# Optimization experiments

Hardware: AMD Instinct MI355X
Metric: run time of the kernel (lower is better)

Reference implementation:

```python
import jax, jax.numpy as jnp
import numpy as np

RAD = 0.15          # sphere radius (init kwarg)
MIN_DIST = 2.0 * RAD  # two spheres collide when center distance < 2*rad


def setup_inputs() -> dict:
    key = jax.random.key(0)
    pos = jax.random.normal(key, (64, 1024, 3), dtype=jnp.float32)  # [T, N, 3]
    return {"pos": pos}


def reference(pos):
    """Sphere collision check equivalent to the sweep-and-prune CUDA kernel.

    The CUDA kernel sorts along one axis purely as an acceleration structure;
    the math it computes is: over all unordered robot pairs (i<j) at each
    timestep, a pair collides if ||p_i - p_j|| < 2*rad. Returns
      count: total number of colliding pairs (int)
      loss:  sum over colliding pairs of (2*rad - dist)^2 penetration penalty
    """
    T, N, _ = pos.shape
    diff = pos[:, :, None, :] - pos[:, None, :, :]          # [T, N, N, 3]
    dist2 = jnp.sum(diff * diff, axis=-1)                   # [T, N, N]
    iu = jnp.triu(jnp.ones((N, N), dtype=bool), k=1)        # i < j, exclude self
    colliding = iu[None, :, :] & (dist2 < MIN_DIST * MIN_DIST)
    # safe sqrt (diagonal / coincident points have dist2 == 0)
    safe_d2 = jnp.where(dist2 > 0.0, dist2, 1.0)
    dist = jnp.sqrt(safe_d2)
    pen = MIN_DIST - dist                                   # penetration depth
    loss = jnp.sum(jnp.where(colliding, pen * pen, 0.0))
    count = jnp.sum(colliding).astype(jnp.int32)
    return (count, loss)
```

## Files before the change

### kernel.cpp

```cpp
#include <hip/hip_runtime.h>
#include <math.h>

#define TN     64
#define NP     1024
#define RADIUS 0.15f
#define MIN_D  (2.0f * RADIUS)
#define R2     (MIN_D * MIN_D)

#define SPLIT  16
#define GI     16
#define NGRP   (NP / GI)
#define GPB    (NGRP / SPLIT)
#define BLOCK  256
#define NBLK   (TN * SPLIT)

__launch_bounds__(BLOCK, 4)
__global__ void collide_kernel(const float* __restrict__ pos,
                               float* __restrict__ partial) {
    __shared__ float sh[NP * 3];
    const int t     = blockIdx.x / SPLIT;
    const int split = blockIdx.x % SPLIT;
    const int tid   = threadIdx.x;

    const float4* p4  = (const float4*)(pos + (size_t)t * NP * 3);
    float4*       sh4 = (float4*)sh;
    #pragma unroll
    for (int i = 0; i < (NP * 3 / 4) / BLOCK; ++i)
        sh4[tid + i * BLOCK] = p4[tid + i * BLOCK];
    __syncthreads();

    unsigned int cnt = 0;
    float loss = 0.0f;

    #pragma unroll
    for (int m = 0; m < GPB; ++m) {
        const int g = (m & 1) ? (m * SPLIT + (SPLIT - 1 - split))
                              : (m * SPLIT + split);
        const int b = g * GI;

        float xi[GI], yi[GI], zi[GI];
        #pragma unroll
        for (int k = 0; k < GI; ++k) {
            xi[k] = sh[3 * (b + k) + 0];
            yi[k] = sh[3 * (b + k) + 1];
            zi[k] = sh[3 * (b + k) + 2];
        }
        #pragma unroll
        for (int k = 0; k < GI; ++k)
            asm volatile("" : "+v"(xi[k]), "+v"(yi[k]), "+v"(zi[k]));

        if (tid < GI - 1) {
            const int j = b + 1 + tid;
            const float xj = sh[3 * j], yj = sh[3 * j + 1], zj = sh[3 * j + 2];
            #pragma unroll
            for (int k = 0; k < GI; ++k) {
                if (k <= tid) {
                    const float dx = xi[k] - xj;
                    const float dy = yi[k] - yj;
                    const float dz = zi[k] - zj;
                    const float d2 = dx * dx + dy * dy + dz * dz;
                    if (d2 < R2) {
                        cnt++;
                        const float pen = MIN_D - __builtin_amdgcn_sqrtf(d2);
                        loss += pen * pen;
                    }
                }
            }
        }

        for (int j = b + GI + tid; j < NP; j += BLOCK) {
            const float xj = sh[3 * j], yj = sh[3 * j + 1], zj = sh[3 * j + 2];
            #pragma unroll
            for (int k = 0; k < GI; ++k) {
                const float dx = xi[k] - xj;
                const float dy = yi[k] - yj;
                const float dz = zi[k] - zj;
                const float d2 = dx * dx + dy * dy + dz * dz;
                const bool hit = d2 < R2;
                cnt += hit ? 1u : 0u;
                if (hit) {
                    const float pen = MIN_D - __builtin_amdgcn_sqrtf(d2);
                    loss += pen * pen;
                }
            }
        }
    }

    float fcnt = (float)cnt;
    #pragma unroll
    for (int off = 32; off > 0; off >>= 1) {
        fcnt += __shfl_down(fcnt, off);
        loss += __shfl_down(loss, off);
    }
    __shared__ float cs[BLOCK / 64], ls[BLOCK / 64];
    const int wave = tid >> 6;
    if ((tid & 63) == 0) { cs[wave] = fcnt; ls[wave] = loss; }
    __syncthreads();
    if (tid == 0) {
        float c = 0.0f, l = 0.0f;
        #pragma unroll
        for (int w = 0; w < BLOCK / 64; ++w) { c += cs[w]; l += ls[w]; }
        partial[2 * blockIdx.x + 0] = c;
        partial[2 * blockIdx.x + 1] = l;
    }
}

__global__ void finalize_kernel(const float* __restrict__ partial,
                                float* __restrict__ out) {
    const int tid = threadIdx.x;
    float c = 0.0f, l = 0.0f;
    #pragma unroll
    for (int i = 0; i < NBLK / BLOCK; ++i) {
        const float2 p = ((const float2*)partial)[tid + i * BLOCK];
        c += p.x;
        l += p.y;
    }
    #pragma unroll
    for (int off = 32; off > 0; off >>= 1) {
        c += __shfl_down(c, off);
        l += __shfl_down(l, off);
    }
    __shared__ float cs[BLOCK / 64], ls[BLOCK / 64];
    const int wave = tid >> 6;
    if ((tid & 63) == 0) { cs[wave] = c; ls[wave] = l; }
    __syncthreads();
    if (tid == 0) {
        float ct = 0.0f, lt = 0.0f;
        #pragma unroll
        for (int w = 0; w < BLOCK / 64; ++w) { ct += cs[w]; lt += ls[w]; }
        out[0] = ct;
        out[1] = lt;
    }
}

extern "C" void kernel_launch(void* const* d_in, const int* in_sizes, int n_in,
                              void* d_out, int out_size, void* d_ws, size_t ws_size,
                              hipStream_t stream) {
    const float* pos     = (const float*)d_in[0];
    float*       partial = (float*)d_ws;
    float*       out     = (float*)d_out;

    collide_kernel<<<NBLK, BLOCK, 0, stream>>>(pos, partial);
    finalize_kernel<<<1, BLOCK, 0, stream>>>(partial, out);
}
```

Before: 73.68 us.

## Bin-sort spheres along x and prune pair checks to neighboring bins

```diff
diff --git a/kernel.cpp b/kernel.cpp
--- a/kernel.cpp
+++ b/kernel.cpp
@@ -7,54 +7,102 @@
 #define MIN_D  (2.0f * RADIUS)
 #define R2     (MIN_D * MIN_D)
 
-#define SPLIT  16
+#define BLOCK  512
+#define WAVES  (BLOCK / 64)
+#define SPLIT  8
 #define GI     16
 #define NGRP   (NP / GI)
-#define GPB    (NGRP / SPLIT)
-#define BLOCK  256
 #define NBLK   (TN * SPLIT)
+#define PPT    (NP / BLOCK)
+
+#define NB     40
+#define XMIN   (-6.0f)
+#define INVW   3.3f
 
 __launch_bounds__(BLOCK, 4)
 __global__ void collide_kernel(const float* __restrict__ pos,
-                               float* __restrict__ partial) {
-    __shared__ float sh[NP * 3];
+                               double* __restrict__ partial) {
+    __shared__ float         shin[NP * 3];
+    __shared__ float         shs [NP * 3];
+    __shared__ unsigned int  hist[NB];
+    __shared__ unsigned int  S[NB + 1];
+    __shared__ unsigned char sbin[NP];
+
     const int t     = blockIdx.x / SPLIT;
     const int split = blockIdx.x % SPLIT;
     const int tid   = threadIdx.x;
+    const int lane  = tid & 63;
+    const int wave  = tid >> 6;
 
     const float4* p4  = (const float4*)(pos + (size_t)t * NP * 3);
-    float4*       sh4 = (float4*)sh;
-    #pragma unroll
-    for (int i = 0; i < (NP * 3 / 4) / BLOCK; ++i)
-        sh4[tid + i * BLOCK] = p4[tid + i * BLOCK];
+    float4*       sh4 = (float4*)shin;
+    for (int i = tid; i < NP * 3 / 4; i += BLOCK) sh4[i] = p4[i];
+    if (tid < NB) hist[tid] = 0u;
     __syncthreads();
 
-    unsigned int cnt = 0;
-    float loss = 0.0f;
+    int          bq[PPT];
+    unsigned int rq[PPT];
+    #pragma unroll
+    for (int q = 0; q < PPT; ++q) {
+        const int p = tid + q * BLOCK;
+        const float x = shin[3 * p];
+        int b = (int)((x - XMIN) * INVW);
+        b = b < 0 ? 0 : (b > NB - 1 ? NB - 1 : b);
+        bq[q] = b;
+        rq[q] = atomicAdd(&hist[b], 1u);
+    }
+    __syncthreads();
+
+    if (tid < 64) {
+        unsigned int c    = (tid < NB) ? hist[tid] : 0u;
+        unsigned int incl = c;
+        #pragma unroll
+        for (int d = 1; d < 64; d <<= 1) {
+            const unsigned int y = __shfl_up(incl, d, 64);
+            if (lane >= d) incl += y;
+        }
+        if (tid < NB) S[tid + 1] = incl;
+        if (tid == 0) S[0] = 0u;
+    }
+    __syncthreads();
 
     #pragma unroll
-    for (int m = 0; m < GPB; ++m) {
-        const int g = (m & 1) ? (m * SPLIT + (SPLIT - 1 - split))
-                              : (m * SPLIT + split);
+    for (int q = 0; q < PPT; ++q) {
+        const int p = tid + q * BLOCK;
+        const unsigned int dst = S[bq[q]] + rq[q];
+        shs[3 * dst + 0] = shin[3 * p + 0];
+        shs[3 * dst + 1] = shin[3 * p + 1];
+        shs[3 * dst + 2] = shin[3 * p + 2];
+        sbin[dst] = (unsigned char)bq[q];
+    }
+    __syncthreads();
+
+    unsigned int cnt  = 0;
+    double       loss = 0.0;
+    {
+        const int g = wave * SPLIT + split;
         const int b = g * GI;
 
         float xi[GI], yi[GI], zi[GI];
         #pragma unroll
         for (int k = 0; k < GI; ++k) {
-            xi[k] = sh[3 * (b + k) + 0];
-            yi[k] = sh[3 * (b + k) + 1];
-            zi[k] = sh[3 * (b + k) + 2];
+            xi[k] = shs[3 * (b + k) + 0];
+            yi[k] = shs[3 * (b + k) + 1];
+            zi[k] = shs[3 * (b + k) + 2];
         }
         #pragma unroll
         for (int k = 0; k < GI; ++k)
             asm volatile("" : "+v"(xi[k]), "+v"(yi[k]), "+v"(zi[k]));
 
-        if (tid < GI - 1) {
-            const int j = b + 1 + tid;
-            const float xj = sh[3 * j], yj = sh[3 * j + 1], zj = sh[3 * j + 2];
+        const int bb   = (int)sbin[b + GI - 1];
+        const int jend = (int)S[(bb + 2 <= NB) ? (bb + 2) : NB];
+
+        if (lane < GI - 1) {
+            const int j = b + 1 + lane;
+            const float xj = shs[3 * j], yj = shs[3 * j + 1], zj = shs[3 * j + 2];
             #pragma unroll
             for (int k = 0; k < GI; ++k) {
-                if (k <= tid) {
+                if (k <= lane) {
                     const float dx = xi[k] - xj;
                     const float dy = yi[k] - yj;
                     const float dz = zi[k] - zj;
@@ -62,14 +110,14 @@
                     if (d2 < R2) {
                         cnt++;
                         const float pen = MIN_D - __builtin_amdgcn_sqrtf(d2);
-                        loss += pen * pen;
+                        loss += (double)(pen * pen);
                     }
                 }
             }
         }
 
-        for (int j = b + GI + tid; j < NP; j += BLOCK) {
-            const float xj = sh[3 * j], yj = sh[3 * j + 1], zj = sh[3 * j + 2];
+        for (int j = b + GI + lane; j < jend; j += 64) {
+            const float xj = shs[3 * j], yj = shs[3 * j + 1], zj = shs[3 * j + 2];
             #pragma unroll
             for (int k = 0; k < GI; ++k) {
                 const float dx = xi[k] - xj;
@@ -80,7 +128,7 @@
                 cnt += hit ? 1u : 0u;
                 if (hit) {
                     const float pen = MIN_D - __builtin_amdgcn_sqrtf(d2);
-                    loss += pen * pen;
+                    loss += (double)(pen * pen);
                 }
             }
         }
@@ -92,26 +140,25 @@
         fcnt += __shfl_down(fcnt, off);
         loss += __shfl_down(loss, off);
     }
-    __shared__ float cs[BLOCK / 64], ls[BLOCK / 64];
-    const int wave = tid >> 6;
-    if ((tid & 63) == 0) { cs[wave] = fcnt; ls[wave] = loss; }
+    __shared__ double cs[WAVES], ls[WAVES];
+    if (lane == 0) { cs[wave] = (double)fcnt; ls[wave] = loss; }
     __syncthreads();
     if (tid == 0) {
-        float c = 0.0f, l = 0.0f;
+        double c = 0.0, l = 0.0;
         #pragma unroll
-        for (int w = 0; w < BLOCK / 64; ++w) { c += cs[w]; l += ls[w]; }
+        for (int w = 0; w < WAVES; ++w) { c += cs[w]; l += ls[w]; }
         partial[2 * blockIdx.x + 0] = c;
         partial[2 * blockIdx.x + 1] = l;
     }
 }
 
-__global__ void finalize_kernel(const float* __restrict__ partial,
+__global__ void finalize_kernel(const double* __restrict__ partial,
                                 float* __restrict__ out) {
     const int tid = threadIdx.x;
-    float c = 0.0f, l = 0.0f;
+    double c = 0.0, l = 0.0;
     #pragma unroll
-    for (int i = 0; i < NBLK / BLOCK; ++i) {
-        const float2 p = ((const float2*)partial)[tid + i * BLOCK];
+    for (int i = 0; i < NBLK / 256; ++i) {
+        const double2 p = ((const double2*)partial)[tid + i * 256];
         c += p.x;
         l += p.y;
     }
@@ -120,16 +167,16 @@
         c += __shfl_down(c, off);
         l += __shfl_down(l, off);
     }
-    __shared__ float cs[BLOCK / 64], ls[BLOCK / 64];
+    __shared__ double cs[4], ls[4];
     const int wave = tid >> 6;
     if ((tid & 63) == 0) { cs[wave] = c; ls[wave] = l; }
     __syncthreads();
     if (tid == 0) {
-        float ct = 0.0f, lt = 0.0f;
+        double ct = 0.0, lt = 0.0;
         #pragma unroll
-        for (int w = 0; w < BLOCK / 64; ++w) { ct += cs[w]; lt += ls[w]; }
-        out[0] = ct;
-        out[1] = lt;
+        for (int w = 0; w < 4; ++w) { ct += cs[w]; lt += ls[w]; }
+        out[0] = (float)ct;
+        out[1] = (float)lt;
     }
 }
 
@@ -137,9 +184,9 @@
                               void* d_out, int out_size, void* d_ws, size_t ws_size,
                               hipStream_t stream) {
     const float* pos     = (const float*)d_in[0];
-    float*       partial = (float*)d_ws;
+    double*      partial = (double*)d_ws;
     float*       out     = (float*)d_out;
 
     collide_kernel<<<NBLK, BLOCK, 0, stream>>>(pos, partial);
-    finalize_kernel<<<1, BLOCK, 0, stream>>>(partial, out);
+    finalize_kernel<<<1, 256, 0, stream>>>(partial, out);
 }
```

Result: faster. 65.36 us (-11.3%).
